# Optimization experiments

Hardware: AMD Instinct MI355X
Metric: run time of the kernel (lower is better)

## Reference

```python
import jax, jax.numpy as jnp
import numpy as np

B, H, S, W, F = 16, 4, 8, 256, 16


def setup_inputs() -> dict:
    key = jax.random.key(0)
    kx, kk = jax.random.split(key)
    x = jax.random.normal(kx, (B, S, W, F), dtype=jnp.float32)
    kernel = jax.random.normal(kk, (H, S, S, W), dtype=jnp.float32)
    return {"x": x, "kernel": kernel}


def reference(x, kernel):
    # kernel: [H, S, S, W]; x: [B, S, W, F]
    Hh, Ss, _, Ww = kernel.shape
    r = jnp.arange(Ww)
    # stacked[h,x,y,j,i] = roll(kernel, shifts=j+1)[i] = kernel[(i-(j+1)) % W]
    idx = (r[None, :] - (r[:, None] + 1)) % Ww          # [W(row=j), W(col=i)]
    stacked = kernel[..., idx]                            # [H,S,S,W,W]
    # torch.tril over last two dims: keep col i <= row j
    tri = (r[None, :] <= r[:, None])                      # [W,W]
    stacked = jnp.where(tri, stacked, jnp.zeros((), dtype=stacked.dtype))
    # masked triangular time-mix contraction
    out = jnp.einsum('hxyji,bxif->bhxyjf', stacked, x)    # [B,H,S,S,W,F]
    base = jnp.arange(1, Ww + 1, dtype=out.dtype).reshape(1, 1, 1, 1, Ww, 1)
    out = out / base
    # transform_x: on diagonal series (x==y) roll time dim by 1, zero first step
    diag_mod = jnp.roll(out, 1, axis=4)
    not_first = (r != 0).reshape(1, 1, 1, 1, Ww, 1)
    diag_mod = diag_mod * not_first.astype(out.dtype)
    eye = jnp.eye(Ss, dtype=bool).reshape(1, 1, Ss, Ss, 1, 1)
    return jnp.where(eye, diag_mod, out)
```

## Files before the change

### kernel.cpp

```cpp
#include <hip/hip_runtime.h>
#include <hip/hip_bf16.h>

typedef short short8 __attribute__((ext_vector_type(8)));
typedef float f32x4 __attribute__((ext_vector_type(4)));

union FragAB { unsigned long long l[2]; int i[4]; short8 v; };

__global__ __launch_bounds__(256, 3)
void k_fused(const float* __restrict__ x,
             const float* __restrict__ kern,
             float* __restrict__ out)
{
    __shared__ __align__(16) ushort Xts[64 * 264];
    __shared__ __align__(8)  ushort wforL[4][336];
    __shared__ float rtab[256];

    const int blk = blockIdx.x;
    const int hy = blk & 31;
    const int sx = (blk >> 5) & 7;
    const int nt = blk >> 8;
    const int h = hy >> 3, sy = hy & 7;
    const int diag = (sx == sy) ? 1 : 0;
    const int t = threadIdx.x;

    {
        const float* krow = kern + ((h * 8 + sx) * 8 + sy) * 256;
        #pragma unroll
        for (int s = 0; s < 4; ++s) {
            #pragma unroll
            for (int pass = 0; pass < 2; ++pass) {
                int q = t + pass * 256;
                if (q < 336) {
                    int src = q - s;
                    float v = (src >= 0 && src < 256) ? krow[src] : 0.0f;
                    __hip_bfloat16 hv = __float2bfloat16(v);
                    wforL[s][q] = reinterpret_cast<ushort&>(hv);
                }
            }
        }
    }
    {
        int denom = t + 1 - diag;
        rtab[t] = (denom > 0) ? (1.0f / (float)denom) : 0.0f;
    }
    {
        const float4* xbase = reinterpret_cast<const float4*>(x);
        #pragma unroll
        for (int it = 0; it < 8; ++it) {
            int id = it * 256 + t;
            int fq = id & 3;
            int k2 = (id >> 2) & 127;
            int bl = id >> 9;
            const float4* rowp = xbase + ((size_t)((nt * 4 + bl) * 8 + sx)) * 1024;
            float4 a = rowp[(2 * k2) * 4 + fq];
            float4 cq = rowp[(2 * k2 + 1) * 4 + fq];
            #pragma unroll
            for (int e = 0; e < 4; ++e) {
                float va = (&a.x)[e], vb = (&cq.x)[e];
                __hip_bfloat16 ha = __float2bfloat16(va);
                __hip_bfloat16 hb = __float2bfloat16(vb);
                uint u = (uint)reinterpret_cast<ushort&>(ha) |
                         ((uint)reinterpret_cast<ushort&>(hb) << 16);
                int row = bl * 16 + fq * 4 + e;
                *reinterpret_cast<uint*>(reinterpret_cast<char*>(Xts) + row * 528 + k2 * 4) = u;
            }
        }
    }
    __syncthreads();

    const int lane = t & 63, wid = t >> 6;
    const int laneM = lane & 15, laneG = lane >> 4;
    const int wj0 = wid * 64;
    const int kmax = wj0 + 64;

    const char* XtsB = reinterpret_cast<const char*>(Xts);
    const char* WB = reinterpret_cast<const char*>(wforL);
    const int abyte = laneM * 528 + laneG * 16;

    const int w00 = 255 + diag - wj0 - laneM + 8 * laneG;
    const int s = (laneM - diag + 1) & 3;
    const int bB = s * 674 + 2 * w00;

    f32x4 acc[4][4];
    #pragma unroll
    for (int m = 0; m < 4; ++m)
        #pragma unroll
        for (int n = 0; n < 4; ++n)
            acc[m][n] = (f32x4){0.0f, 0.0f, 0.0f, 0.0f};

    for (int kc = 0; kc < kmax; kc += 32) {
        FragAB af[4];
        #pragma unroll
        for (int m = 0; m < 4; ++m) {
            const int4 raw = *reinterpret_cast<const int4*>(XtsB + abyte + m * 8448 + kc * 2);
            af[m].i[0] = raw.x; af[m].i[1] = raw.y;
            af[m].i[2] = raw.z; af[m].i[3] = raw.w;
        }
        FragAB bf[4];
        #pragma unroll
        for (int n = 0; n < 4; ++n) {
            const char* p = WB + bB + kc * 2 - 32 * n;
            bf[n].l[0] = *reinterpret_cast<const unsigned long long*>(p);
            bf[n].l[1] = *reinterpret_cast<const unsigned long long*>(p + 8);
        }
        #pragma unroll
        for (int m = 0; m < 4; ++m)
            #pragma unroll
            for (int n = 0; n < 4; ++n)
                acc[m][n] = __builtin_amdgcn_mfma_f32_16x16x32_bf16(
                    af[m].v, bf[n].v, acc[m][n], 0, 0, 0);
    }

    #pragma unroll
    for (int m = 0; m < 4; ++m) {
        const int b_ = nt * 4 + m;
        float* obase = out + (((size_t)(b_ * 4 + h) * 8 + sx) * 8 + sy) * 4096
                       + laneG * 4;
        #pragma unroll
        for (int n = 0; n < 4; ++n) {
            const int j = wj0 + 16 * n + laneM;
            const float rt = rtab[j];
            float4 v;
            v.x = acc[m][n][0] * rt;
            v.y = acc[m][n][1] * rt;
            v.z = acc[m][n][2] * rt;
            v.w = acc[m][n][3] * rt;
            *reinterpret_cast<float4*>(obase + (size_t)j * 16) = v;
        }
    }
}

extern "C" void kernel_launch(void* const* d_in, const int* in_sizes, int n_in,
                              void* d_out, int out_size, void* d_ws, size_t ws_size,
                              hipStream_t stream) {
    const float* x    = (const float*)d_in[0];
    const float* kern = (const float*)d_in[1];
    float* out = (float*)d_out;

    k_fused<<<1024, 256, 0, stream>>>(x, kern, out);
}
```

Before: 20.92 us.

## Tighten triangular K bound per output sub-tile and interleave stores with compute

Restructures the MFMA loop so each 16-column output sub-tile runs its own K loop, bounded by that sub-tile's triangular extent instead of the whole wave's 64-column range. This skips MFMA work on fully masked zero blocks. It also cuts live accumulators from 16 to 4 so occupancy can rise to 4 blocks per CU, and each sub-tile's results are stored with nontemporal stores as soon as they are ready. In exchange, A fragments are reloaded from LDS once per sub-tile, which raises LDS traffic.

```diff
diff --git a/kernel.cpp b/kernel.cpp
--- a/kernel.cpp
+++ b/kernel.cpp
@@ -6,7 +6,7 @@
 
 union FragAB { unsigned long long l[2]; int i[4]; short8 v; };
 
-__global__ __launch_bounds__(256, 3)
+__global__ __launch_bounds__(256, 4)
 void k_fused(const float* __restrict__ x,
              const float* __restrict__ kern,
              float* __restrict__ out)
@@ -71,7 +71,6 @@
     const int lane = t & 63, wid = t >> 6;
     const int laneM = lane & 15, laneG = lane >> 4;
     const int wj0 = wid * 64;
-    const int kmax = wj0 + 64;
 
     const char* XtsB = reinterpret_cast<const char*>(Xts);
     const char* WB = reinterpret_cast<const char*>(wforL);
@@ -81,51 +80,43 @@
     const int s = (laneM - diag + 1) & 3;
     const int bB = s * 674 + 2 * w00;
 
-    f32x4 acc[4][4];
     #pragma unroll
-    for (int m = 0; m < 4; ++m)
+    for (int n = 0; n < 4; ++n) {
+        const int kmaxn = wj0 + 16 * (n + 1);
+
+        f32x4 acc[4];
         #pragma unroll
-        for (int n = 0; n < 4; ++n)
-            acc[m][n] = (f32x4){0.0f, 0.0f, 0.0f, 0.0f};
+        for (int m = 0; m < 4; ++m) acc[m] = (f32x4){0.0f, 0.0f, 0.0f, 0.0f};
 
-    for (int kc = 0; kc < kmax; kc += 32) {
-        FragAB af[4];
+        for (int kc = 0; kc < kmaxn; kc += 32) {
+            FragAB bf;
+            {
+                const char* p = WB + bB + kc * 2 - 32 * n;
+                bf.l[0] = *reinterpret_cast<const unsigned long long*>(p);
+                bf.l[1] = *reinterpret_cast<const unsigned long long*>(p + 8);
+            }
+            FragAB af[4];
+            #pragma unroll
+            for (int m = 0; m < 4; ++m) {
+                const int4 raw = *reinterpret_cast<const int4*>(XtsB + abyte + m * 8448 + kc * 2);
+                af[m].i[0] = raw.x; af[m].i[1] = raw.y;
+                af[m].i[2] = raw.z; af[m].i[3] = raw.w;
+            }
+            #pragma unroll
+            for (int m = 0; m < 4; ++m)
+                acc[m] = __builtin_amdgcn_mfma_f32_16x16x32_bf16(
+                    af[m].v, bf.v, acc[m], 0, 0, 0);
+        }
+
+        const int j = wj0 + 16 * n + laneM;
+        const float rt = rtab[j];
         #pragma unroll
         for (int m = 0; m < 4; ++m) {
-            const int4 raw = *reinterpret_cast<const int4*>(XtsB + abyte + m * 8448 + kc * 2);
-            af[m].i[0] = raw.x; af[m].i[1] = raw.y;
-            af[m].i[2] = raw.z; af[m].i[3] = raw.w;
-        }
-        FragAB bf[4];
-        #pragma unroll
-        for (int n = 0; n < 4; ++n) {
-            const char* p = WB + bB + kc * 2 - 32 * n;
-            bf[n].l[0] = *reinterpret_cast<const unsigned long long*>(p);
-            bf[n].l[1] = *reinterpret_cast<const unsigned long long*>(p + 8);
-        }
-        #pragma unroll
-        for (int m = 0; m < 4; ++m)
-            #pragma unroll
-            for (int n = 0; n < 4; ++n)
-                acc[m][n] = __builtin_amdgcn_mfma_f32_16x16x32_bf16(
-                    af[m].v, bf[n].v, acc[m][n], 0, 0, 0);
-    }
-
-    #pragma unroll
-    for (int m = 0; m < 4; ++m) {
-        const int b_ = nt * 4 + m;
-        float* obase = out + (((size_t)(b_ * 4 + h) * 8 + sx) * 8 + sy) * 4096
-                       + laneG * 4;
-        #pragma unroll
-        for (int n = 0; n < 4; ++n) {
-            const int j = wj0 + 16 * n + laneM;
-            const float rt = rtab[j];
-            float4 v;
-            v.x = acc[m][n][0] * rt;
-            v.y = acc[m][n][1] * rt;
-            v.z = acc[m][n][2] * rt;
-            v.w = acc[m][n][3] * rt;
-            *reinterpret_cast<float4*>(obase + (size_t)j * 16) = v;
+            const int b_ = nt * 4 + m;
+            float* dst = out + (((size_t)(b_ * 4 + h) * 8 + sx) * 8 + sy) * 4096
+                         + (size_t)j * 16 + laneG * 4;
+            f32x4 v = acc[m] * rt;
+            __builtin_nontemporal_store(v, reinterpret_cast<f32x4*>(dst));
         }
     }
 }
```

Measured after the change: 22.59 us. 1.08x slower.
